# Kernel tuning notes

Hardware: AMD Instinct MI355X
Metric: run time of the kernel (lower is better)

## Reference

```python
import jax, jax.numpy as jnp
import numpy as np

NLAYERS = 4
HEADS = 4
HEAD_DIM = 64
C = HEADS * HEAD_DIM  # 256
MAX_LEN = 1024


def setup_inputs() -> dict:
    key = jax.random.key(0)
    k1, k2, k3 = jax.random.split(key, 3)
    B, S = 16, 1024
    x = jax.random.normal(k1, (B, C, 1, S), dtype=jnp.float32)
    # length is only used via its static shape[0]; values are irrelevant
    length = jnp.zeros((MAX_LEN,), dtype=jnp.int32)
    # per-layer 1x1 conv weights, std=0.1 as in the torch init (squeeze the 1x1 spatial dims)
    w = jax.random.normal(k2, (NLAYERS, C, C), dtype=jnp.float32) * 0.1
    # persistent kv buffer
    kv = jax.random.normal(k3, (NLAYERS, HEADS, MAX_LEN, HEAD_DIM), dtype=jnp.float32) * 0.1
    return {"x": x, "length": length, "w": w, "kv": kv}


def reference(x, length, w, kv):
    B, _, _, S = x.shape
    L = length.shape[0]  # static slice length into kv buffer
    scale = 1.0 / jnp.sqrt(jnp.asarray(HEAD_DIM, dtype=x.dtype))
    for i in range(NLAYERS):
        # 1x1 conv == channel projection: (B,C,1,S) -> (B,C,1,S)
        x = jnp.einsum('oc,bchs->bohs', w[i], x)
        # view (B,4,64,S) then permute -> query (B,H,S,D)
        q = x.reshape(B, HEADS, HEAD_DIM, S).transpose(0, 1, 3, 2)
        kvi = kv[i, :, :L]  # (H, L, D); broadcasts over batch like the (1,H,L,D) torch slice
        # scaled dot-product attention with k == v == kvi
        scores = jnp.einsum('bhsd,hld->bhsl', q, kvi) * scale
        attn = jax.nn.softmax(scores, axis=-1)
        o = jnp.einsum('bhsl,hld->bhsd', attn, kvi)  # (B,H,S,D)
        # permute back and merge heads -> (B,256,1,S)
        x = o.transpose(0, 1, 3, 2).reshape(B, C, 1, S)
    return x
```

## Files before the change

### kernel.cpp

```cpp
#include <hip/hip_runtime.h>

#define NL   4
#define NH   4
#define HD   64
#define CD   256
#define SQL  1024
#define BB   16

typedef _Float16 half8 __attribute__((ext_vector_type(8)));
typedef _Float16 half4 __attribute__((ext_vector_type(4)));
typedef _Float16 half2v __attribute__((ext_vector_type(2)));
typedef float    f32x4 __attribute__((ext_vector_type(4)));
typedef unsigned short u16x8 __attribute__((ext_vector_type(8)));

static __device__ __forceinline__ float bf2f(unsigned short u) {
    union { unsigned int i; float f; } v; v.i = ((unsigned int)u) << 16; return v.f;
}
static __device__ __forceinline__ unsigned short f2bf(float f) {
    union { float f; unsigned int i; } v; v.f = f;
    unsigned int u = v.i;
    return (unsigned short)((u + 0x7fffu + ((u >> 16) & 1u)) >> 16);
}

static __device__ __forceinline__ int detect_flag(const void* win) {
    const unsigned int* w = (const unsigned int*)win;
    int cnt = 0;
#pragma unroll 1
    for (int i = 0; i < 64; i++) {
        unsigned int lo = w[i] & 0xFFFFu;
        int e = (int)((lo >> 7) & 0xFF);
        cnt += (e >= 96 && e <= 144) ? 1 : 0;
    }
    return cnt >= 48 ? 1 : 0;
}

__global__ __launch_bounds__(256) void prep_all(const void* __restrict__ xin,
                                                const void* __restrict__ win,
                                                const void* __restrict__ kvin,
                                                _Float16* __restrict__ x16,
                                                _Float16* __restrict__ w16,
                                                _Float16* __restrict__ kaF,
                                                _Float16* __restrict__ vtF) {
    __shared__ __align__(16) _Float16 tile[64][72];
    const int bi = blockIdx.x;
    const int t = threadIdx.x;
    const int isbf = detect_flag(win);

    if (bi < 1024) {
        const int st = bi & 15, ct = (bi >> 4) & 3, b = bi >> 6;
        const int r = t >> 2, seg = t & 3;
        const size_t base = ((size_t)(b * CD + ct * 64 + r)) * SQL + st * 64 + seg * 16;
        float v[16];
        if (isbf) {
            const unsigned short* src = (const unsigned short*)xin + base;
            u16x8 u0 = *(const u16x8*)(src);
            u16x8 u1 = *(const u16x8*)(src + 8);
#pragma unroll
            for (int j = 0; j < 8; j++) { v[j] = bf2f(u0[j]); v[8 + j] = bf2f(u1[j]); }
        } else {
            const float* src = (const float*)xin + base;
#pragma unroll
            for (int c = 0; c < 4; c++) {
                f32x4 a = *(const f32x4*)(src + c * 4);
#pragma unroll
                for (int j = 0; j < 4; j++) v[c * 4 + j] = a[j];
            }
        }
#pragma unroll
        for (int j = 0; j < 16; j++) tile[r][seg * 16 + j] = (_Float16)v[j];
        __syncthreads();
        half8 o0, o1;
#pragma unroll
        for (int j = 0; j < 8; j++) { o0[j] = tile[seg * 16 + j][r]; o1[j] = tile[seg * 16 + 8 + j][r]; }
        _Float16* dt = x16 + ((size_t)(b * SQL + st * 64 + r)) * CD + ct * 64 + seg * 16;
        *(half8*)(dt) = o0;
        *(half8*)(dt + 8) = o1;
    } else if (bi < 1280) {
        const int j2 = bi - 1024;
        const int lt = j2 & 15, ih = j2 >> 4;
        const int r = t >> 2, seg = t & 3;
        const size_t base = ((size_t)(ih * SQL + lt * 64 + r)) * HD + seg * 16;
        float v[16];
        if (isbf) {
            const unsigned short* src = (const unsigned short*)kvin + base;
            u16x8 u0 = *(const u16x8*)(src);
            u16x8 u1 = *(const u16x8*)(src + 8);
#pragma unroll
            for (int j = 0; j < 8; j++) { v[j] = bf2f(u0[j]); v[8 + j] = bf2f(u1[j]); }
        } else {
            const float* src = (const float*)kvin + base;
#pragma unroll
            for (int c = 0; c < 4; c++) {
                f32x4 a = *(const f32x4*)(src + c * 4);
#pragma unroll
                for (int j = 0; j < 4; j++) v[c * 4 + j] = a[j];
            }
        }
#pragma unroll
        for (int j = 0; j < 16; j++) tile[r][seg * 16 + j] = (_Float16)v[j];
        __syncthreads();
        const int l = t & 63, l16 = l & 15, q = l >> 4;
        _Float16* kaB = kaF + ((size_t)ih << 16);
        _Float16* vtB = vtF + ((size_t)ih << 16);
#pragma unroll
        for (int it = 0; it < 2; it++) {
            const int c = (t >> 6) + it * 4;
            const int kd = c >> 1, msp = c & 1;
            half8 ok, ov;
#pragma unroll
            for (int j = 0; j < 4; j++) {
                ok[j]     = tile[msp * 32 + l16][kd * 16 + q * 4 + j];
                ok[4 + j] = tile[msp * 32 + 16 + l16][kd * 16 + q * 4 + j];
                ov[j]     = tile[kd * 16 + q * 4 + j][msp * 32 + l16];
                ov[4 + j] = tile[kd * 16 + q * 4 + j][msp * 32 + 16 + l16];
            }
            *(half8*)(kaB + ((lt * 8 + c) << 9) + l * 8) = ok;
            *(half8*)(vtB + ((lt * 8 + c) << 9) + l * 8) = ov;
        }
    } else {
        const int i = (bi - 1280) * 256 + t;
        const size_t base = (size_t)i * 8;
        half8 h;
        if (isbf) {
            u16x8 u = *(const u16x8*)((const unsigned short*)win + base);
#pragma unroll
            for (int j = 0; j < 8; j++) h[j] = (_Float16)bf2f(u[j]);
        } else {
            const float* p = (const float*)win + base;
            f32x4 a0 = *(const f32x4*)(p);
            f32x4 a1 = *(const f32x4*)(p + 4);
#pragma unroll
            for (int j = 0; j < 4; j++) { h[j] = (_Float16)a0[j]; h[4 + j] = (_Float16)a1[j]; }
        }
        *(half8*)(w16 + base) = h;
    }
}

__global__ __launch_bounds__(256, 4) void layer_fused(const _Float16* __restrict__ xg,
                                                      _Float16* __restrict__ xout,
                                                      const _Float16* __restrict__ w16,
                                                      const _Float16* __restrict__ kaF,
                                                      const _Float16* __restrict__ vtF,
                                                      const void* __restrict__ win,
                                                      void* __restrict__ outp,
                                                      int L) {
    __shared__ __align__(16) _Float16 kvbuf[2][8192];
    const int sb = blockIdx.x;
    const int h  = blockIdx.y;
    const int b  = blockIdx.z;
    const int t  = threadIdx.x;
    const int wv = t >> 6, lane = t & 63, l16 = lane & 15, quad = lane >> 4;
    const int s0 = sb * 64 + wv * 16;

    const _Float16* kaB = kaF + ((size_t)(L * NH + h) << 16);
    const _Float16* vtB = vtF + ((size_t)(L * NH + h) << 16);

    auto stage = [&](int lt, int buf) {
#pragma unroll
        for (int j = 0; j < 4; j++) {
            const int c = wv * 4 + j;
            const _Float16* src = (c < 8)
                ? kaB + (((lt * 8 + c) << 9))
                : vtB + (((lt * 8 + (c - 8)) << 9));
            __builtin_amdgcn_global_load_lds(
                (const __attribute__((address_space(1))) void*)(src + lane * 8),
                (__attribute__((address_space(3))) void*)(&kvbuf[buf][c * 512]),
                16, 0, 0);
        }
    };

    stage(0, 0);

    f32x4 gacc[4];
#pragma unroll
    for (int md = 0; md < 4; md++)
#pragma unroll
        for (int r = 0; r < 4; r++) gacc[md][r] = 0.0f;
    const _Float16* wb = w16 + ((size_t)L << 16) + ((size_t)(h * 64) << 8);
#pragma unroll
    for (int kk = 0; kk < 8; kk++) {
        half8 bx = *(const half8*)(xg + ((size_t)((b << 10) + s0 + l16) << 8) +
                                   kk * 32 + quad * 8);
#pragma unroll
        for (int md = 0; md < 4; md++) {
            half8 aw = *(const half8*)(wb + ((size_t)(md * 16 + l16) << 8) + kk * 32 + quad * 8);
            gacc[md] = __builtin_amdgcn_mfma_f32_16x16x32_f16(aw, bx, gacc[md], 0, 0, 0);
        }
    }
    half4 qh[4];
#pragma unroll
    for (int md = 0; md < 4; md++)
#pragma unroll
        for (int r = 0; r < 4; r++)
            qh[md][r] = (_Float16)(gacc[md][r] * 0.180336880111120f);

    half4 ones4;
#pragma unroll
    for (int r = 0; r < 4; r++) ones4[r] = (_Float16)1.0f;

    f32x4 oacc[4];
    f32x4 osum;
#pragma unroll
    for (int md = 0; md < 4; md++)
#pragma unroll
        for (int r = 0; r < 4; r++) oacc[md][r] = 0.0f;
#pragma unroll
    for (int r = 0; r < 4; r++) osum[r] = 0.0f;

    __syncthreads();

#pragma unroll 1
    for (int lt = 0; lt < 16; lt++) {
        const int buf = lt & 1;
        if (lt + 1 < 16) stage(lt + 1, buf ^ 1);

        const _Float16* base = &kvbuf[buf][0];
        half8 kab[8], vab[8];
#pragma unroll
        for (int c = 0; c < 8; c++)
            kab[c] = *(const half8*)(base + c * 512 + lane * 8);
#pragma unroll
        for (int c = 0; c < 8; c++)
            vab[c] = *(const half8*)(base + (8 + c) * 512 + lane * 8);

        f32x4 stt[4];
#pragma unroll
        for (int ms = 0; ms < 4; ms++)
#pragma unroll
            for (int r = 0; r < 4; r++) stt[ms][r] = 0.0f;
#pragma unroll
        for (int kd = 0; kd < 4; kd++)
#pragma unroll
            for (int msp = 0; msp < 2; msp++) {
                half8 kk8 = kab[kd * 2 + msp];
                half4 lo = __builtin_shufflevector(kk8, kk8, 0, 1, 2, 3);
                half4 hi = __builtin_shufflevector(kk8, kk8, 4, 5, 6, 7);
                stt[msp * 2] = __builtin_amdgcn_mfma_f32_16x16x16f16(
                    lo, qh[kd], stt[msp * 2], 0, 0, 0);
                stt[msp * 2 + 1] = __builtin_amdgcn_mfma_f32_16x16x16f16(
                    hi, qh[kd], stt[msp * 2 + 1], 0, 0, 0);
            }

        half4 pb[4];
#pragma unroll
        for (int ms = 0; ms < 4; ms++) {
            float e0 = __builtin_amdgcn_exp2f(stt[ms][0]);
            float e1 = __builtin_amdgcn_exp2f(stt[ms][1]);
            float e2 = __builtin_amdgcn_exp2f(stt[ms][2]);
            float e3 = __builtin_amdgcn_exp2f(stt[ms][3]);
            half2v p01 = __builtin_bit_cast(half2v, __builtin_amdgcn_cvt_pkrtz(e0, e1));
            half2v p23 = __builtin_bit_cast(half2v, __builtin_amdgcn_cvt_pkrtz(e2, e3));
            pb[ms] = __builtin_shufflevector(p01, p23, 0, 1, 2, 3);
        }

#pragma unroll
        for (int ks = 0; ks < 4; ks++) {
            osum = __builtin_amdgcn_mfma_f32_16x16x16f16(ones4, pb[ks], osum, 0, 0, 0);
#pragma unroll
            for (int mdp = 0; mdp < 2; mdp++) {
                half8 vv8 = vab[ks * 2 + mdp];
                half4 lo = __builtin_shufflevector(vv8, vv8, 0, 1, 2, 3);
                half4 hi = __builtin_shufflevector(vv8, vv8, 4, 5, 6, 7);
                oacc[mdp * 2] = __builtin_amdgcn_mfma_f32_16x16x16f16(
                    lo, pb[ks], oacc[mdp * 2], 0, 0, 0);
                oacc[mdp * 2 + 1] = __builtin_amdgcn_mfma_f32_16x16x16f16(
                    hi, pb[ks], oacc[mdp * 2 + 1], 0, 0, 0);
            }
        }
        __syncthreads();
    }

    const float inv = 1.0f / osum[0];
    const int s = s0 + l16;

    if (L < NL - 1) {
#pragma unroll
        for (int md = 0; md < 4; md++) {
            half4 hv;
#pragma unroll
            for (int r = 0; r < 4; r++) hv[r] = (_Float16)(oacc[md][r] * inv);
            *(half4*)(xout + (((size_t)((b << 10) + s)) << 8) + (h << 6) + md * 16 + quad * 4) = hv;
        }
    } else if (detect_flag(win)) {
#pragma unroll
        for (int md = 0; md < 4; md++) {
#pragma unroll
            for (int r = 0; r < 4; r++) {
                const int c = (h << 6) + md * 16 + quad * 4 + r;
                ((unsigned short*)outp)[(((size_t)(b * CD + c)) << 10) + s] =
                    f2bf(oacc[md][r] * inv);
            }
        }
    } else {
#pragma unroll
        for (int md = 0; md < 4; md++) {
#pragma unroll
            for (int r = 0; r < 4; r++) {
                const int c = (h << 6) + md * 16 + quad * 4 + r;
                ((float*)outp)[(((size_t)(b * CD + c)) << 10) + s] =
                    oacc[md][r] * inv;
            }
        }
    }
}

extern "C" void kernel_launch(void* const* d_in, const int* in_sizes, int n_in,
                              void* d_out, int out_size, void* d_ws, size_t ws_size,
                              hipStream_t stream) {
    const void* xin = d_in[0];
    const void* win = d_in[2];
    const void* kvin = d_in[3];

    char* ws = (char*)d_ws;
    const size_t MB = 1u << 20;
    _Float16* xa  = (_Float16*)(ws);
    _Float16* xb  = (_Float16*)(ws + 8 * MB);
    _Float16* w16 = (_Float16*)(ws + 16 * MB);
    _Float16* kaF = (_Float16*)(ws + 17 * MB);
    _Float16* vtF = (_Float16*)(ws + 19 * MB);

    prep_all<<<dim3(1024 + 256 + 128), 256, 0, stream>>>(xin, win, kvin, xa, w16, kaF, vtF);

    _Float16* cur = xa;
    _Float16* nxt = xb;
    for (int i = 0; i < NL; i++) {
        layer_fused<<<dim3(SQL / 64, NH, BB), 256, 0, stream>>>(cur, nxt, w16, kaF, vtF,
                                                                win, d_out, i);
        _Float16* tmp = cur; cur = nxt; nxt = tmp;
    }
}
```

Baseline: 242.6 us.

## Switch attention to 32x32x16 MFMA with 128-query blocks and permlane swaps

Rewrites the fused layer kernel to use 32x32x16 f16 MFMA instructions, with each wave handling 32 queries and each block 128. The K/V tiles are repacked in the prep kernel to match the new operand layout, and two tiles are staged per double-buffer step. The row sum is now taken from the exponentials in vector ALU instead of an extra ones-MFMA, and permlane32 swaps convert accumulator layout into operand layout. The goal is fewer MFMA issues and more K/V reuse per LDS load, at the cost of higher register pressure (occupancy hint lowered from 4 to 2) and a grid half as large.

After: 204.4 us. -15.8%, faster.

```diff
diff --git a/kernel.cpp b/kernel.cpp
--- a/kernel.cpp
+++ b/kernel.cpp
@@ -11,7 +11,9 @@
 typedef _Float16 half4 __attribute__((ext_vector_type(4)));
 typedef _Float16 half2v __attribute__((ext_vector_type(2)));
 typedef float    f32x4 __attribute__((ext_vector_type(4)));
+typedef float    f32x16 __attribute__((ext_vector_type(16)));
 typedef unsigned short u16x8 __attribute__((ext_vector_type(8)));
+typedef unsigned int  uint4v __attribute__((ext_vector_type(4)));
 
 static __device__ __forceinline__ float bf2f(unsigned short u) {
     union { unsigned int i; float f; } v; v.i = ((unsigned int)u) << 16; return v.f;
@@ -99,21 +101,17 @@
 #pragma unroll
         for (int j = 0; j < 16; j++) tile[r][seg * 16 + j] = (_Float16)v[j];
         __syncthreads();
-        const int l = t & 63, l16 = l & 15, q = l >> 4;
+        const int l = t & 63, hie = l >> 5, lne = l & 31;
         _Float16* kaB = kaF + ((size_t)ih << 16);
         _Float16* vtB = vtF + ((size_t)ih << 16);
 #pragma unroll
         for (int it = 0; it < 2; it++) {
             const int c = (t >> 6) + it * 4;
-            const int kd = c >> 1, msp = c & 1;
-            half8 ok, ov;
-#pragma unroll
-            for (int j = 0; j < 4; j++) {
-                ok[j]     = tile[msp * 32 + l16][kd * 16 + q * 4 + j];
-                ok[4 + j] = tile[msp * 32 + 16 + l16][kd * 16 + q * 4 + j];
-                ov[j]     = tile[kd * 16 + q * 4 + j][msp * 32 + l16];
-                ov[4 + j] = tile[kd * 16 + q * 4 + j][msp * 32 + 16 + l16];
-            }
+            half8 ok = *(const half8*)(&tile[(c >> 2) * 32 + lne][(c & 3) * 16 + hie * 8]);
+            half8 ov;
+#pragma unroll
+            for (int j = 0; j < 8; j++)
+                ov[j] = tile[(c & 3) * 16 + hie * 8 + j][(c >> 2) * 32 + lne];
             *(half8*)(kaB + ((lt * 8 + c) << 9) + l * 8) = ok;
             *(half8*)(vtB + ((lt * 8 + c) << 9) + l * 8) = ov;
         }
@@ -136,7 +134,7 @@
     }
 }
 
-__global__ __launch_bounds__(256, 4) void layer_fused(const _Float16* __restrict__ xg,
+__global__ __launch_bounds__(256, 2) void layer_fused(const _Float16* __restrict__ xg,
                                                       _Float16* __restrict__ xout,
                                                       const _Float16* __restrict__ w16,
                                                       const _Float16* __restrict__ kaF,
@@ -144,18 +142,18 @@
                                                       const void* __restrict__ win,
                                                       void* __restrict__ outp,
                                                       int L) {
-    __shared__ __align__(16) _Float16 kvbuf[2][8192];
+    __shared__ __align__(16) _Float16 kvbuf[2][16384];
     const int sb = blockIdx.x;
     const int h  = blockIdx.y;
     const int b  = blockIdx.z;
     const int t  = threadIdx.x;
-    const int wv = t >> 6, lane = t & 63, l16 = lane & 15, quad = lane >> 4;
-    const int s0 = sb * 64 + wv * 16;
+    const int wv = t >> 6, lane = t & 63, ln = lane & 31, hi = lane >> 5;
+    const int s0 = sb * 128 + wv * 32;
 
     const _Float16* kaB = kaF + ((size_t)(L * NH + h) << 16);
     const _Float16* vtB = vtF + ((size_t)(L * NH + h) << 16);
 
-    auto stage = [&](int lt, int buf) {
+    auto stage = [&](int lt, int buf, int hf) {
 #pragma unroll
         for (int j = 0; j < 4; j++) {
             const int c = wv * 4 + j;
@@ -164,143 +162,171 @@
                 : vtB + (((lt * 8 + (c - 8)) << 9));
             __builtin_amdgcn_global_load_lds(
                 (const __attribute__((address_space(1))) void*)(src + lane * 8),
-                (__attribute__((address_space(3))) void*)(&kvbuf[buf][c * 512]),
+                (__attribute__((address_space(3))) void*)(&kvbuf[buf][hf * 8192 + c * 512]),
                 16, 0, 0);
         }
     };
 
-    stage(0, 0);
-
-    f32x4 gacc[4];
-#pragma unroll
-    for (int md = 0; md < 4; md++)
-#pragma unroll
-        for (int r = 0; r < 4; r++) gacc[md][r] = 0.0f;
+    stage(0, 0, 0);
+    stage(1, 0, 1);
+
+    f32x16 gacc[2];
+#pragma unroll
+    for (int dblk = 0; dblk < 2; dblk++)
+#pragma unroll
+        for (int r = 0; r < 16; r++) gacc[dblk][r] = 0.0f;
     const _Float16* wb = w16 + ((size_t)L << 16) + ((size_t)(h * 64) << 8);
 #pragma unroll
-    for (int kk = 0; kk < 8; kk++) {
-        half8 bx = *(const half8*)(xg + ((size_t)((b << 10) + s0 + l16) << 8) +
-                                   kk * 32 + quad * 8);
-#pragma unroll
-        for (int md = 0; md < 4; md++) {
-            half8 aw = *(const half8*)(wb + ((size_t)(md * 16 + l16) << 8) + kk * 32 + quad * 8);
-            gacc[md] = __builtin_amdgcn_mfma_f32_16x16x32_f16(aw, bx, gacc[md], 0, 0, 0);
-        }
-    }
-    half4 qh[4];
-#pragma unroll
-    for (int md = 0; md < 4; md++)
-#pragma unroll
-        for (int r = 0; r < 4; r++)
-            qh[md][r] = (_Float16)(gacc[md][r] * 0.180336880111120f);
-
-    half4 ones4;
-#pragma unroll
-    for (int r = 0; r < 4; r++) ones4[r] = (_Float16)1.0f;
-
-    f32x4 oacc[4];
-    f32x4 osum;
-#pragma unroll
-    for (int md = 0; md < 4; md++)
-#pragma unroll
-        for (int r = 0; r < 4; r++) oacc[md][r] = 0.0f;
-#pragma unroll
-    for (int r = 0; r < 4; r++) osum[r] = 0.0f;
+    for (int kc = 0; kc < 16; kc++) {
+        half8 bx = *(const half8*)(xg + ((size_t)((b << 10) + s0 + ln) << 8) + kc * 16 + hi * 8);
+#pragma unroll
+        for (int dblk = 0; dblk < 2; dblk++) {
+            half8 aw = *(const half8*)(wb + ((size_t)(dblk * 32 + ln) << 8) + kc * 16 + hi * 8);
+            gacc[dblk] = __builtin_amdgcn_mfma_f32_32x32x16_f16(aw, bx, gacc[dblk], 0, 0, 0);
+        }
+    }
+
+    const float sc = 0.180336880111120f;
+    half8 qb[4];
+#pragma unroll
+    for (int dblk = 0; dblk < 2; dblk++)
+#pragma unroll
+        for (int k1 = 0; k1 < 2; k1++) {
+            unsigned int u01 = __builtin_bit_cast(unsigned int,
+                __builtin_amdgcn_cvt_pkrtz(gacc[dblk][k1 * 8 + 0] * sc, gacc[dblk][k1 * 8 + 1] * sc));
+            unsigned int u23 = __builtin_bit_cast(unsigned int,
+                __builtin_amdgcn_cvt_pkrtz(gacc[dblk][k1 * 8 + 2] * sc, gacc[dblk][k1 * 8 + 3] * sc));
+            unsigned int w01 = __builtin_bit_cast(unsigned int,
+                __builtin_amdgcn_cvt_pkrtz(gacc[dblk][k1 * 8 + 4] * sc, gacc[dblk][k1 * 8 + 5] * sc));
+            unsigned int w23 = __builtin_bit_cast(unsigned int,
+                __builtin_amdgcn_cvt_pkrtz(gacc[dblk][k1 * 8 + 6] * sc, gacc[dblk][k1 * 8 + 7] * sc));
+            asm("v_permlane32_swap_b32 %0, %1" : "+v"(u01), "+v"(w01));
+            asm("v_permlane32_swap_b32 %0, %1" : "+v"(u23), "+v"(w23));
+            uint4v q; q[0] = u01; q[1] = u23; q[2] = w01; q[3] = w23;
+            qb[dblk * 2 + k1] = __builtin_bit_cast(half8, q);
+        }
+
+    f32x16 oacc[2];
+#pragma unroll
+    for (int dblk = 0; dblk < 2; dblk++)
+#pragma unroll
+        for (int r = 0; r < 16; r++) oacc[dblk][r] = 0.0f;
+    f32x4 rsum;
+#pragma unroll
+    for (int r = 0; r < 4; r++) rsum[r] = 0.0f;
 
     __syncthreads();
 
 #pragma unroll 1
-    for (int lt = 0; lt < 16; lt++) {
-        const int buf = lt & 1;
-        if (lt + 1 < 16) stage(lt + 1, buf ^ 1);
-
-        const _Float16* base = &kvbuf[buf][0];
-        half8 kab[8], vab[8];
-#pragma unroll
-        for (int c = 0; c < 8; c++)
-            kab[c] = *(const half8*)(base + c * 512 + lane * 8);
-#pragma unroll
-        for (int c = 0; c < 8; c++)
-            vab[c] = *(const half8*)(base + (8 + c) * 512 + lane * 8);
-
-        f32x4 stt[4];
-#pragma unroll
-        for (int ms = 0; ms < 4; ms++)
-#pragma unroll
-            for (int r = 0; r < 4; r++) stt[ms][r] = 0.0f;
-#pragma unroll
-        for (int kd = 0; kd < 4; kd++)
-#pragma unroll
-            for (int msp = 0; msp < 2; msp++) {
-                half8 kk8 = kab[kd * 2 + msp];
-                half4 lo = __builtin_shufflevector(kk8, kk8, 0, 1, 2, 3);
-                half4 hi = __builtin_shufflevector(kk8, kk8, 4, 5, 6, 7);
-                stt[msp * 2] = __builtin_amdgcn_mfma_f32_16x16x16f16(
-                    lo, qh[kd], stt[msp * 2], 0, 0, 0);
-                stt[msp * 2 + 1] = __builtin_amdgcn_mfma_f32_16x16x16f16(
-                    hi, qh[kd], stt[msp * 2 + 1], 0, 0, 0);
+    for (int ltp = 0; ltp < 8; ltp++) {
+        const int buf = ltp & 1;
+        if (ltp < 7) { stage(2 * ltp + 2, buf ^ 1, 0); stage(2 * ltp + 3, buf ^ 1, 1); }
+#pragma unroll
+        for (int sub = 0; sub < 2; sub++) {
+            const _Float16* base = &kvbuf[buf][sub * 8192];
+            half8 kab[8];
+#pragma unroll
+            for (int c = 0; c < 8; c++)
+                kab[c] = *(const half8*)(base + c * 512 + lane * 8);
+
+            f32x16 stt[2];
+#pragma unroll
+            for (int lblk = 0; lblk < 2; lblk++)
+#pragma unroll
+                for (int r = 0; r < 16; r++) stt[lblk][r] = 0.0f;
+            __builtin_amdgcn_s_setprio(1);
+#pragma unroll
+            for (int lblk = 0; lblk < 2; lblk++)
+#pragma unroll
+                for (int kd = 0; kd < 4; kd++)
+                    stt[lblk] = __builtin_amdgcn_mfma_f32_32x32x16_f16(
+                        kab[lblk * 4 + kd], qb[kd], stt[lblk], 0, 0, 0);
+            __builtin_amdgcn_s_setprio(0);
+
+            half8 vab[8];
+#pragma unroll
+            for (int c = 0; c < 8; c++)
+                vab[c] = *(const half8*)(base + (8 + c) * 512 + lane * 8);
+
+            half8 pb[4];
+#pragma unroll
+            for (int lblk = 0; lblk < 2; lblk++) {
+                float e[16];
+#pragma unroll
+                for (int r = 0; r < 16; r++) e[r] = __builtin_amdgcn_exp2f(stt[lblk][r]);
+#pragma unroll
+                for (int g = 0; g < 4; g++)
+                    rsum[g] += (e[g * 4 + 0] + e[g * 4 + 1]) + (e[g * 4 + 2] + e[g * 4 + 3]);
+#pragma unroll
+                for (int k1 = 0; k1 < 2; k1++) {
+                    unsigned int u01 = __builtin_bit_cast(unsigned int,
+                        __builtin_amdgcn_cvt_pkrtz(e[k1 * 8 + 0], e[k1 * 8 + 1]));
+                    unsigned int u23 = __builtin_bit_cast(unsigned int,
+                        __builtin_amdgcn_cvt_pkrtz(e[k1 * 8 + 2], e[k1 * 8 + 3]));
+                    unsigned int w01 = __builtin_bit_cast(unsigned int,
+                        __builtin_amdgcn_cvt_pkrtz(e[k1 * 8 + 4], e[k1 * 8 + 5]));
+                    unsigned int w23 = __builtin_bit_cast(unsigned int,
+                        __builtin_amdgcn_cvt_pkrtz(e[k1 * 8 + 6], e[k1 * 8 + 7]));
+                    asm("v_permlane32_swap_b32 %0, %1" : "+v"(u01), "+v"(w01));
+                    asm("v_permlane32_swap_b32 %0, %1" : "+v"(u23), "+v"(w23));
+                    uint4v p; p[0] = u01; p[1] = u23; p[2] = w01; p[3] = w23;
+                    pb[lblk * 2 + k1] = __builtin_bit_cast(half8, p);
+                }
             }
 
-        half4 pb[4];
-#pragma unroll
-        for (int ms = 0; ms < 4; ms++) {
-            float e0 = __builtin_amdgcn_exp2f(stt[ms][0]);
-            float e1 = __builtin_amdgcn_exp2f(stt[ms][1]);
-            float e2 = __builtin_amdgcn_exp2f(stt[ms][2]);
-            float e3 = __builtin_amdgcn_exp2f(stt[ms][3]);
-            half2v p01 = __builtin_bit_cast(half2v, __builtin_amdgcn_cvt_pkrtz(e0, e1));
-            half2v p23 = __builtin_bit_cast(half2v, __builtin_amdgcn_cvt_pkrtz(e2, e3));
-            pb[ms] = __builtin_shufflevector(p01, p23, 0, 1, 2, 3);
-        }
-
-#pragma unroll
-        for (int ks = 0; ks < 4; ks++) {
-            osum = __builtin_amdgcn_mfma_f32_16x16x16f16(ones4, pb[ks], osum, 0, 0, 0);
-#pragma unroll
-            for (int mdp = 0; mdp < 2; mdp++) {
-                half8 vv8 = vab[ks * 2 + mdp];
-                half4 lo = __builtin_shufflevector(vv8, vv8, 0, 1, 2, 3);
-                half4 hi = __builtin_shufflevector(vv8, vv8, 4, 5, 6, 7);
-                oacc[mdp * 2] = __builtin_amdgcn_mfma_f32_16x16x16f16(
-                    lo, pb[ks], oacc[mdp * 2], 0, 0, 0);
-                oacc[mdp * 2 + 1] = __builtin_amdgcn_mfma_f32_16x16x16f16(
-                    hi, pb[ks], oacc[mdp * 2 + 1], 0, 0, 0);
+            __builtin_amdgcn_s_setprio(1);
+#pragma unroll
+            for (int dblk = 0; dblk < 2; dblk++)
+#pragma unroll
+                for (int ks = 0; ks < 4; ks++)
+                    oacc[dblk] = __builtin_amdgcn_mfma_f32_32x32x16_f16(
+                        vab[dblk * 4 + ks], pb[ks], oacc[dblk], 0, 0, 0);
+            __builtin_amdgcn_s_setprio(0);
+        }
+        __syncthreads();
+    }
+
+    float rs = (rsum[0] + rsum[1]) + (rsum[2] + rsum[3]);
+    unsigned int ra = __builtin_bit_cast(unsigned int, rs);
+    unsigned int rb = ra;
+    asm("" : "+v"(rb));
+    asm("v_permlane32_swap_b32 %0, %1" : "+v"(ra), "+v"(rb));
+    const float inv = 1.0f / (__builtin_bit_cast(float, ra) + __builtin_bit_cast(float, rb));
+    const int s = s0 + ln;
+
+    if (L < NL - 1) {
+#pragma unroll
+        for (int dblk = 0; dblk < 2; dblk++)
+#pragma unroll
+            for (int q2 = 0; q2 < 4; q2++) {
+                half4 hv;
+#pragma unroll
+                for (int r = 0; r < 4; r++) hv[r] = (_Float16)(oacc[dblk][q2 * 4 + r] * inv);
+                *(half4*)(xout + (((size_t)((b << 10) + s)) << 8) +
+                          (h << 6) + dblk * 32 + q2 * 8 + hi * 4) = hv;
             }
-        }
-        __syncthreads();
-    }
-
-    const float inv = 1.0f / osum[0];
-    const int s = s0 + l16;
-
-    if (L < NL - 1) {
-#pragma unroll
-        for (int md = 0; md < 4; md++) {
-            half4 hv;
-#pragma unroll
-            for (int r = 0; r < 4; r++) hv[r] = (_Float16)(oacc[md][r] * inv);
-            *(half4*)(xout + (((size_t)((b << 10) + s)) << 8) + (h << 6) + md * 16 + quad * 4) = hv;
-        }
     } else if (detect_flag(win)) {
 #pragma unroll
-        for (int md = 0; md < 4; md++) {
-#pragma unroll
-            for (int r = 0; r < 4; r++) {
-                const int c = (h << 6) + md * 16 + quad * 4 + r;
-                ((unsigned short*)outp)[(((size_t)(b * CD + c)) << 10) + s] =
-                    f2bf(oacc[md][r] * inv);
-            }
-        }
+        for (int dblk = 0; dblk < 2; dblk++)
+#pragma unroll
+            for (int q2 = 0; q2 < 4; q2++)
+#pragma unroll
+                for (int r = 0; r < 4; r++) {
+                    const int c = (h << 6) + dblk * 32 + q2 * 8 + hi * 4 + r;
+                    ((unsigned short*)outp)[(((size_t)(b * CD + c)) << 10) + s] =
+                        f2bf(oacc[dblk][q2 * 4 + r] * inv);
+                }
     } else {
 #pragma unroll
-        for (int md = 0; md < 4; md++) {
-#pragma unroll
-            for (int r = 0; r < 4; r++) {
-                const int c = (h << 6) + md * 16 + quad * 4 + r;
-                ((float*)outp)[(((size_t)(b * CD + c)) << 10) + s] =
-                    oacc[md][r] * inv;
-            }
-        }
+        for (int dblk = 0; dblk < 2; dblk++)
+#pragma unroll
+            for (int q2 = 0; q2 < 4; q2++)
+#pragma unroll
+                for (int r = 0; r < 4; r++) {
+                    const int c = (h << 6) + dblk * 32 + q2 * 8 + hi * 4 + r;
+                    ((float*)outp)[(((size_t)(b * CD + c)) << 10) + s] =
+                        oacc[dblk][q2 * 4 + r] * inv;
+                }
     }
 }
 
@@ -324,8 +350,8 @@
     _Float16* cur = xa;
     _Float16* nxt = xb;
     for (int i = 0; i < NL; i++) {
-        layer_fused<<<dim3(SQL / 64, NH, BB), 256, 0, stream>>>(cur, nxt, w16, kaF, vtF,
-                                                                win, d_out, i);
+        layer_fused<<<dim3(SQL / 128, NH, BB), 256, 0, stream>>>(cur, nxt, w16, kaF, vtF,
+                                                                 win, d_out, i);
         _Float16* tmp = cur; cur = nxt; nxt = tmp;
     }
 }
```
